# Optimization experiments

Measured on AMD Instinct MI355X. Metric: run time of the kernel, lower is better.

Reference implementation:

```python
import jax, jax.numpy as jnp
import numpy as np

N_NODES = 10000
N_EDGES = 320000
IN_DIM = 128
HID = 256


def setup_inputs() -> dict:
    key = jax.random.key(0)
    ks = jax.random.split(key, 10)
    s_in = 1.0 / np.sqrt(IN_DIM)
    s_h = 1.0 / np.sqrt(HID)
    return {
        "x": jax.random.normal(ks[0], (N_NODES, IN_DIM), dtype=jnp.float32),
        "edge_index": jax.random.randint(ks[1], (2, N_EDGES), 0, N_NODES, dtype=jnp.int64),
        # feature_projector Linear(IN_DIM -> HID)
        "Wp": jax.random.uniform(ks[2], (IN_DIM, HID), jnp.float32, -s_in, s_in),
        "bp": jax.random.uniform(ks[3], (HID,), jnp.float32, -s_in, s_in),
        # LSTM(input=HID, hidden=HID) params, torch layout [4H, H], gate order i,f,g,o
        "W_ih": jax.random.uniform(ks[4], (4 * HID, HID), jnp.float32, -s_h, s_h),
        "W_hh": jax.random.uniform(ks[5], (4 * HID, HID), jnp.float32, -s_h, s_h),
        "b_ih": jax.random.uniform(ks[6], (4 * HID,), jnp.float32, -s_h, s_h),
        "b_hh": jax.random.uniform(ks[7], (4 * HID,), jnp.float32, -s_h, s_h),
        # EvolveGCN-O initial weight [H, H] (glorot-style)
        "initial_weight": jax.random.normal(ks[8], (HID, HID), dtype=jnp.float32) * np.sqrt(2.0 / (2 * HID)),
        # GCNConv bias
        "b_gcn": jnp.zeros((HID,), dtype=jnp.float32),
    }


def _forward(x, edge_index, Wp, bp, W_ih, W_hh, b_ih, b_hh, initial_weight, b_gcn):
    n = x.shape[0]
    # 1) feature projection
    h = x @ Wp + bp  # [N, H]
    # 2) EvolveGCN-O: one LSTM step on the weight matrix (rows = batch),
    #    with h0 = c0 = initial_weight; evolved hidden state is the GCN weight.
    gates = initial_weight @ W_ih.T + b_ih + initial_weight @ W_hh.T + b_hh  # [H, 4H]
    i_g, f_g, g_g, o_g = jnp.split(gates, 4, axis=-1)
    c = jax.nn.sigmoid(f_g) * initial_weight + jax.nn.sigmoid(i_g) * jnp.tanh(g_g)
    W = jax.nn.sigmoid(o_g) * jnp.tanh(c)  # [H, H]
    # 3) GCN propagation with fixed W: out = D^{-1/2}(A+I)D^{-1/2} (h W) + b
    hw = h @ W  # [N, H]
    self_loop = jnp.arange(n, dtype=edge_index.dtype)
    src = jnp.concatenate([edge_index[0], self_loop])
    dst = jnp.concatenate([edge_index[1], self_loop])
    ones = jnp.ones(src.shape[0], dtype=hw.dtype)
    deg = jax.ops.segment_sum(ones, dst, num_segments=n)  # in-degree incl. self loop
    dinv = jnp.where(deg > 0, jax.lax.rsqrt(deg), 0.0)
    norm = dinv[src] * dinv[dst]  # [E+N]
    out = jax.ops.segment_sum(hw[src] * norm[:, None], dst, num_segments=n)
    return out + b_gcn


def reference(x, edge_index, Wp, bp, W_ih, W_hh, b_ih, b_hh, initial_weight, b_gcn):
    return _forward(x, edge_index, Wp, bp, W_ih, W_hh, b_ih, b_hh, initial_weight, b_gcn)
```

## Files before the change

### kernel.cpp

```cpp
#include <hip/hip_runtime.h>
#include <math.h>

#define N_NODES 10000
#define N_EDGES 320000
#define IN_DIM  128
#define HID     256
#define CAP     128

#define NB_GATES 128
#define NB_FILL  313
#define NB_XCVT  80

typedef __attribute__((ext_vector_type(8))) short frag_ab;
typedef __attribute__((ext_vector_type(4))) float frag_cd;


__device__ __forceinline__ unsigned bf16rne(float f) {
    union { float f; unsigned u; } c; c.f = f;
    return (c.u + 0x7FFFu + ((c.u >> 16) & 1u)) >> 16;
}

__global__ __launch_bounds__(256)
void k_prep(const int* __restrict__ ei, int* __restrict__ cursor,
            int* __restrict__ bucket, const float* __restrict__ iw,
            const float* __restrict__ wih, const float* __restrict__ whh,
            float* __restrict__ G) {
    __shared__ float smem[6144];
    if (blockIdx.x >= NB_GATES) {
        int e = ((blockIdx.x - NB_GATES) * 256 + threadIdx.x) * 4;
        if (e + 3 < N_EDGES) {
            int4 s4 = *(const int4*)&ei[e];
            int4 d4 = *(const int4*)&ei[N_EDGES + e];
            int p0 = atomicAdd(&cursor[d4.x], 1);
            if (p0 < CAP) bucket[d4.x * CAP + p0] = s4.x;
            int p1 = atomicAdd(&cursor[d4.y], 1);
            if (p1 < CAP) bucket[d4.y * CAP + p1] = s4.y;
            int p2 = atomicAdd(&cursor[d4.z], 1);
            if (p2 < CAP) bucket[d4.z * CAP + p2] = s4.z;
            int p3 = atomicAdd(&cursor[d4.w], 1);
            if (p3 < CAP) bucket[d4.w * CAP + p3] = s4.w;
        } else {
            for (int q = e; q < N_EDGES; ++q) {
                int s = ei[q];
                int d = ei[N_EDGES + q];
                int pos = atomicAdd(&cursor[d], 1);
                if (pos < CAP) bucket[d * CAP + pos] = s;
            }
        }
        return;
    }
    int bid = blockIdx.x;
    int m0 = (bid & 7) * 32, n0 = (bid >> 3) * 64;
    float (*aT)[32] = (float(*)[32])smem;
    float (*bS)[64] = (float(*)[64])(smem + 2048);
    int t = threadIdx.x;
    int tm = t & 15, tn = t >> 4;
    float acc[2][4] = {};
    for (int kt = 0; kt < 4; ++kt) {
        int k0 = kt * 64;
        {
            int row = t >> 3;
            #pragma unroll
            for (int r = 0; r < 2; ++r) {
                int kq = 2 * (t & 7) + r;
                float4 av = *(const float4*)&iw[(m0 + row) * HID + k0 + 4 * kq];
                aT[4 * kq + 0][row] = av.x; aT[4 * kq + 1][row] = av.y;
                aT[4 * kq + 2][row] = av.z; aT[4 * kq + 3][row] = av.w;
            }
        }
        {
            int row = t >> 2;
            #pragma unroll
            for (int r = 0; r < 4; ++r) {
                int kq = 4 * (t & 3) + r;
                float4 b1 = *(const float4*)&wih[(n0 + row) * HID + k0 + 4 * kq];
                float4 b2 = *(const float4*)&whh[(n0 + row) * HID + k0 + 4 * kq];
                bS[4 * kq + 0][row] = b1.x + b2.x; bS[4 * kq + 1][row] = b1.y + b2.y;
                bS[4 * kq + 2][row] = b1.z + b2.z; bS[4 * kq + 3][row] = b1.w + b2.w;
            }
        }
        __syncthreads();
        #pragma unroll 8
        for (int kk = 0; kk < 64; ++kk) {
            float2 a2 = *(const float2*)&aT[kk][2 * tm];
            float4 b4 = *(const float4*)&bS[kk][4 * tn];
            float a[2] = {a2.x, a2.y};
            float b[4] = {b4.x, b4.y, b4.z, b4.w};
            #pragma unroll
            for (int i = 0; i < 2; ++i)
                #pragma unroll
                for (int j = 0; j < 4; ++j)
                    acc[i][j] = fmaf(a[i], b[j], acc[i][j]);
        }
        __syncthreads();
    }
    #pragma unroll
    for (int i = 0; i < 2; ++i) {
        float4 o = make_float4(acc[i][0], acc[i][1], acc[i][2], acc[i][3]);
        *(float4*)&G[(m0 + 2 * tm + i) * 1024 + n0 + 4 * tn] = o;
    }
}

__device__ __forceinline__ float sig_f(float x)  { return 1.f / (1.f + __expf(-x)); }
__device__ __forceinline__ float tanh_f(float x) { return 1.f - 2.f / (1.f + __expf(2.f * x)); }

__global__ __launch_bounds__(256)
void k_wev_dinv_xcvt(const float* __restrict__ G, const float* __restrict__ iw,
                     const float* __restrict__ b_ih, const float* __restrict__ b_hh,
                     float* __restrict__ Wev, const int* __restrict__ cursor,
                     float* __restrict__ dinv, const float* __restrict__ x,
                     unsigned* __restrict__ xb) {
    if (blockIdx.x >= 296) {
        int tid = (blockIdx.x - 296) * 256 + threadIdx.x;
        const float2* x2 = (const float2*)x;
        #pragma unroll
        for (int it = 0; it < 32; ++it) {
            int idx = tid + it * (NB_XCVT * 256);
            if (idx < N_NODES * 64) {
                int v = idx >> 6;
                float dv = rsqrtf((float)(cursor[v] + 1));
                float2 val = x2[idx];
                xb[idx] = bf16rne(dv * val.x) | (bf16rne(dv * val.y) << 16);
            }
        }
        return;
    }
    if (blockIdx.x >= 256) {
        int v = (blockIdx.x - 256) * 256 + threadIdx.x;
        if (v < N_NODES) dinv[v] = rsqrtf((float)(cursor[v] + 1));
        return;
    }
    int r = blockIdx.x;
    int j = threadIdx.x;
    float gi = G[r * 1024 + 0   + j] + b_ih[0   + j] + b_hh[0   + j];
    float gf = G[r * 1024 + 256 + j] + b_ih[256 + j] + b_hh[256 + j];
    float gg = G[r * 1024 + 512 + j] + b_ih[512 + j] + b_hh[512 + j];
    float go = G[r * 1024 + 768 + j] + b_ih[768 + j] + b_hh[768 + j];
    float c  = sig_f(gf) * iw[r * HID + j] + sig_f(gi) * tanh_f(gg);
    Wev[r * HID + j] = sig_f(go) * tanh_f(c);
}

__global__ __launch_bounds__(256)
void k_wc_agg(const unsigned* __restrict__ xb, const int* __restrict__ bucket,
              const int* __restrict__ cursor, const float* __restrict__ dinv,
              unsigned* __restrict__ yb, float* __restrict__ rs,
              const float* __restrict__ Wp, const float* __restrict__ bp,
              const float* __restrict__ Wev, unsigned* __restrict__ wct,
              float* __restrict__ bc) {
    __shared__ float arow[HID];
    if (blockIdx.x < 129) {
        int a = blockIdx.x;
        int j = threadIdx.x;
        const float* srcRow = (a < IN_DIM) ? &Wp[a * HID] : bp;
        arow[j] = srcRow[j];
        __syncthreads();
        float acc = 0.f;
        #pragma unroll 4
        for (int k = 0; k < HID; ++k)
            acc = fmaf(arow[k], Wev[k * HID + j], acc);
        if (a < IN_DIM)
            ((unsigned short*)wct)[j * IN_DIM + a] = (unsigned short)bf16rne(acc);
        else
            bc[j] = acc;
        return;
    }
    int wv   = threadIdx.x >> 6;
    int lane = threadIdx.x & 63;
    int v = (blockIdx.x - 129) * 4 + wv;
    int cntv = cursor[v];
    float dv = dinv[v];
    int cnt = cntv > CAP ? CAP : cntv;
    unsigned self = xb[v * 64 + lane];
    union { unsigned u; float f; } c0, c1;
    c0.u = self << 16; c1.u = self & 0xFFFF0000u;
    float acc0 = c0.f, acc1 = c1.f;
    float wsum = dv;
    const int4* bkt4 = (const int4*)&bucket[v * CAP];
    int j = 0;
    for (; j + 4 <= cnt; j += 4) {
        int4 s = bkt4[j >> 2];
        float w0 = dinv[s.x], w1 = dinv[s.y], w2 = dinv[s.z], w3 = dinv[s.w];
        unsigned r0 = xb[s.x * 64 + lane];
        unsigned r1 = xb[s.y * 64 + lane];
        unsigned r2 = xb[s.z * 64 + lane];
        unsigned r3 = xb[s.w * 64 + lane];
        union { unsigned u; float f; } a0, a1;
        a0.u = r0 << 16; a1.u = r0 & 0xFFFF0000u; acc0 += a0.f; acc1 += a1.f;
        a0.u = r1 << 16; a1.u = r1 & 0xFFFF0000u; acc0 += a0.f; acc1 += a1.f;
        a0.u = r2 << 16; a1.u = r2 & 0xFFFF0000u; acc0 += a0.f; acc1 += a1.f;
        a0.u = r3 << 16; a1.u = r3 & 0xFFFF0000u; acc0 += a0.f; acc1 += a1.f;
        wsum += w0 + w1 + w2 + w3;
    }
    for (; j < cnt; ++j) {
        int s = ((const int*)bkt4)[j];
        wsum += dinv[s];
        unsigned r = xb[s * 64 + lane];
        union { unsigned u; float f; } a0, a1;
        a0.u = r << 16; a1.u = r & 0xFFFF0000u; acc0 += a0.f; acc1 += a1.f;
    }
    yb[v * 64 + lane] = bf16rne(dv * acc0) | (bf16rne(dv * acc1) << 16);
    if (lane == 0) rs[v] = dv * wsum;
}

__global__ __launch_bounds__(256)
void k_out(const unsigned* __restrict__ yb, const unsigned* __restrict__ wct,
           const float* __restrict__ bc, const float* __restrict__ rs,
           const float* __restrict__ b_gcn, float* __restrict__ out) {
    __shared__ float sm[32][260];
    int m0 = blockIdx.x * 32;
    int w = threadIdx.x >> 6, lane = threadIdx.x & 63;
    int q = lane >> 4, ln = lane & 15;
    const int4* yb4  = (const int4*)yb;
    const int4* wct4 = (const int4*)wct;
    union F { int4 v; frag_ab f; };
    F a[2][4];
    #pragma unroll
    for (int mt = 0; mt < 2; ++mt)
        #pragma unroll
        for (int kc = 0; kc < 4; ++kc)
            a[mt][kc].v = yb4[(m0 + mt * 16 + ln) * 16 + kc * 4 + q];
    #pragma unroll
    for (int i = 0; i < 4; ++i) {
        int n0w = w * 64 + i * 16;
        F b[4];
        #pragma unroll
        for (int kc = 0; kc < 4; ++kc)
            b[kc].v = wct4[(n0w + ln) * 16 + kc * 4 + q];
        frag_cd acc0 = {0.f, 0.f, 0.f, 0.f};
        frag_cd acc1 = {0.f, 0.f, 0.f, 0.f};
        #pragma unroll
        for (int kc = 0; kc < 4; ++kc) {
            acc0 = __builtin_amdgcn_mfma_f32_16x16x32_bf16(a[0][kc].f, b[kc].f, acc0, 0, 0, 0);
            acc1 = __builtin_amdgcn_mfma_f32_16x16x32_bf16(a[1][kc].f, b[kc].f, acc1, 0, 0, 0);
        }
        #pragma unroll
        for (int r = 0; r < 4; ++r) {
            sm[q * 4 + r][n0w + ln]      = acc0[r];
            sm[16 + q * 4 + r][n0w + ln] = acc1[r];
        }
    }
    __syncthreads();
    int m  = threadIdx.x >> 3;
    int cg = threadIdx.x & 7;
    int gm = m0 + m;
    if (gm < N_NODES) {
        float rsv = rs[gm];
        #pragma unroll
        for (int c = 0; c < 8; ++c) {
            int col = c * 32 + cg * 4;
            float4 vv  = *(float4*)&sm[m][col];
            float4 bcv = *(const float4*)&bc[col];
            float4 bgv = *(const float4*)&b_gcn[col];
            float4 o;
            o.x = vv.x + rsv * bcv.x + bgv.x;
            o.y = vv.y + rsv * bcv.y + bgv.y;
            o.z = vv.z + rsv * bcv.z + bgv.z;
            o.w = vv.w + rsv * bcv.w + bgv.w;
            *(float4*)&out[gm * HID + col] = o;
        }
    }
}

extern "C" void kernel_launch(void* const* d_in, const int* in_sizes, int n_in,
                              void* d_out, int out_size, void* d_ws, size_t ws_size,
                              hipStream_t stream) {
    const float* x     = (const float*)d_in[0];
    const int*   ei    = (const int*)d_in[1];
    const float* Wp    = (const float*)d_in[2];
    const float* bp    = (const float*)d_in[3];
    const float* W_ih  = (const float*)d_in[4];
    const float* W_hh  = (const float*)d_in[5];
    const float* b_ih  = (const float*)d_in[6];
    const float* b_hh  = (const float*)d_in[7];
    const float* iw    = (const float*)d_in[8];
    const float* b_gcn = (const float*)d_in[9];
    float* out = (float*)d_out;

    char* ws = (char*)d_ws;
    unsigned* yb     = (unsigned*)(ws + 0);
    float*    G      = (float*)   (ws + 2560000);
    float*    Wev    = (float*)   (ws + 3608576);
    unsigned* wct    = (unsigned*)(ws + 3870720);
    float*    bc     = (float*)   (ws + 3936256);
    float*    rs     = (float*)   (ws + 3937280);
    unsigned* xb     = (unsigned*)(ws + 3977280);
    int*      cursor = (int*)     (ws + 6537280);
    float*    dinv   = (float*)   (ws + 6577280);
    int*      bucket = (int*)     (ws + 6617280);

    hipMemsetAsync(cursor, 0, N_NODES * sizeof(int), stream);

    k_prep<<<NB_GATES + NB_FILL, 256, 0, stream>>>(ei, cursor, bucket, iw, W_ih, W_hh, G);
    k_wev_dinv_xcvt<<<256 + 40 + NB_XCVT, 256, 0, stream>>>(
        G, iw, b_ih, b_hh, Wev, cursor, dinv, x, xb);
    k_wc_agg<<<129 + 2500, 256, 0, stream>>>(xb, bucket, cursor, dinv, yb, rs, Wp, bp, Wev, wct, bc);
    k_out<<<313, 256, 0, stream>>>(yb, wct, bc, rs, b_gcn, out);
}
```

Before: 143.7 us.

## Split gate GEMM over K, move x bf16 conversion into prep kernel

The LSTM gate GEMM is split into two K-halves across twice as many blocks, writing partial sums to G and G2, which the Wev kernel then adds. The x-to-bf16 conversion no longer depends on degree, so it moves into the first kernel alongside edge bucketing and runs with many more blocks. The per-source dinv weighting shifts into the aggregation loop as FMAs. This shortens the critical path of the second kernel and spreads work across more CUs, at the cost of an extra partial-sum buffer and one extra multiply per gathered element.

```diff
diff --git a/kernel.cpp b/kernel.cpp
--- a/kernel.cpp
+++ b/kernel.cpp
@@ -7,9 +7,9 @@
 #define HID     256
 #define CAP     128
 
-#define NB_GATES 128
+#define NB_GATES 256
 #define NB_FILL  313
-#define NB_XCVT  80
+#define NB_XCVT  640
 
 typedef __attribute__((ext_vector_type(8))) short frag_ab;
 typedef __attribute__((ext_vector_type(4))) float frag_cd;
@@ -24,8 +24,22 @@
 void k_prep(const int* __restrict__ ei, int* __restrict__ cursor,
             int* __restrict__ bucket, const float* __restrict__ iw,
             const float* __restrict__ wih, const float* __restrict__ whh,
-            float* __restrict__ G) {
+            float* __restrict__ G, float* __restrict__ G2,
+            const float* __restrict__ x, unsigned* __restrict__ xb) {
     __shared__ float smem[6144];
+    if (blockIdx.x >= NB_GATES + NB_FILL) {
+        int tid = (blockIdx.x - NB_GATES - NB_FILL) * 256 + threadIdx.x;
+        const float2* x2 = (const float2*)x;
+        #pragma unroll
+        for (int it = 0; it < 4; ++it) {
+            int idx = tid + it * (NB_XCVT * 256);
+            if (idx < N_NODES * 64) {
+                float2 v = x2[idx];
+                xb[idx] = bf16rne(v.x) | (bf16rne(v.y) << 16);
+            }
+        }
+        return;
+    }
     if (blockIdx.x >= NB_GATES) {
         int e = ((blockIdx.x - NB_GATES) * 256 + threadIdx.x) * 4;
         if (e + 3 < N_EDGES) {
@@ -49,15 +63,18 @@
         }
         return;
     }
-    int bid = blockIdx.x;
-    int m0 = (bid & 7) * 32, n0 = (bid >> 3) * 64;
+    int half = blockIdx.x >> 7;
+    int sub  = blockIdx.x & 127;
+    int m0 = (sub & 7) * 32, n0 = (sub >> 3) * 64;
+    int kbase = half * 128;
+    float* Gh = half ? G2 : G;
     float (*aT)[32] = (float(*)[32])smem;
     float (*bS)[64] = (float(*)[64])(smem + 2048);
     int t = threadIdx.x;
     int tm = t & 15, tn = t >> 4;
     float acc[2][4] = {};
-    for (int kt = 0; kt < 4; ++kt) {
-        int k0 = kt * 64;
+    for (int kt = 0; kt < 2; ++kt) {
+        int k0 = kbase + kt * 64;
         {
             int row = t >> 3;
             #pragma unroll
@@ -97,7 +114,7 @@
     #pragma unroll
     for (int i = 0; i < 2; ++i) {
         float4 o = make_float4(acc[i][0], acc[i][1], acc[i][2], acc[i][3]);
-        *(float4*)&G[(m0 + 2 * tm + i) * 1024 + n0 + 4 * tn] = o;
+        *(float4*)&Gh[(m0 + 2 * tm + i) * 1024 + n0 + 4 * tn] = o;
     }
 }
 
@@ -105,26 +122,10 @@
 __device__ __forceinline__ float tanh_f(float x) { return 1.f - 2.f / (1.f + __expf(2.f * x)); }
 
 __global__ __launch_bounds__(256)
-void k_wev_dinv_xcvt(const float* __restrict__ G, const float* __restrict__ iw,
-                     const float* __restrict__ b_ih, const float* __restrict__ b_hh,
-                     float* __restrict__ Wev, const int* __restrict__ cursor,
-                     float* __restrict__ dinv, const float* __restrict__ x,
-                     unsigned* __restrict__ xb) {
-    if (blockIdx.x >= 296) {
-        int tid = (blockIdx.x - 296) * 256 + threadIdx.x;
-        const float2* x2 = (const float2*)x;
-        #pragma unroll
-        for (int it = 0; it < 32; ++it) {
-            int idx = tid + it * (NB_XCVT * 256);
-            if (idx < N_NODES * 64) {
-                int v = idx >> 6;
-                float dv = rsqrtf((float)(cursor[v] + 1));
-                float2 val = x2[idx];
-                xb[idx] = bf16rne(dv * val.x) | (bf16rne(dv * val.y) << 16);
-            }
-        }
-        return;
-    }
+void k_wev_dinv(const float* __restrict__ G, const float* __restrict__ G2,
+                const float* __restrict__ iw, const float* __restrict__ b_ih,
+                const float* __restrict__ b_hh, float* __restrict__ Wev,
+                const int* __restrict__ cursor, float* __restrict__ dinv) {
     if (blockIdx.x >= 256) {
         int v = (blockIdx.x - 256) * 256 + threadIdx.x;
         if (v < N_NODES) dinv[v] = rsqrtf((float)(cursor[v] + 1));
@@ -132,10 +133,10 @@
     }
     int r = blockIdx.x;
     int j = threadIdx.x;
-    float gi = G[r * 1024 + 0   + j] + b_ih[0   + j] + b_hh[0   + j];
-    float gf = G[r * 1024 + 256 + j] + b_ih[256 + j] + b_hh[256 + j];
-    float gg = G[r * 1024 + 512 + j] + b_ih[512 + j] + b_hh[512 + j];
-    float go = G[r * 1024 + 768 + j] + b_ih[768 + j] + b_hh[768 + j];
+    float gi = G[r * 1024 + 0   + j] + G2[r * 1024 + 0   + j] + b_ih[0   + j] + b_hh[0   + j];
+    float gf = G[r * 1024 + 256 + j] + G2[r * 1024 + 256 + j] + b_ih[256 + j] + b_hh[256 + j];
+    float gg = G[r * 1024 + 512 + j] + G2[r * 1024 + 512 + j] + b_ih[512 + j] + b_hh[512 + j];
+    float go = G[r * 1024 + 768 + j] + G2[r * 1024 + 768 + j] + b_ih[768 + j] + b_hh[768 + j];
     float c  = sig_f(gf) * iw[r * HID + j] + sig_f(gi) * tanh_f(gg);
     Wev[r * HID + j] = sig_f(go) * tanh_f(c);
 }
@@ -173,7 +174,7 @@
     unsigned self = xb[v * 64 + lane];
     union { unsigned u; float f; } c0, c1;
     c0.u = self << 16; c1.u = self & 0xFFFF0000u;
-    float acc0 = c0.f, acc1 = c1.f;
+    float acc0 = dv * c0.f, acc1 = dv * c1.f;
     float wsum = dv;
     const int4* bkt4 = (const int4*)&bucket[v * CAP];
     int j = 0;
@@ -185,18 +186,24 @@
         unsigned r2 = xb[s.z * 64 + lane];
         unsigned r3 = xb[s.w * 64 + lane];
         union { unsigned u; float f; } a0, a1;
-        a0.u = r0 << 16; a1.u = r0 & 0xFFFF0000u; acc0 += a0.f; acc1 += a1.f;
-        a0.u = r1 << 16; a1.u = r1 & 0xFFFF0000u; acc0 += a0.f; acc1 += a1.f;
-        a0.u = r2 << 16; a1.u = r2 & 0xFFFF0000u; acc0 += a0.f; acc1 += a1.f;
-        a0.u = r3 << 16; a1.u = r3 & 0xFFFF0000u; acc0 += a0.f; acc1 += a1.f;
+        a0.u = r0 << 16; a1.u = r0 & 0xFFFF0000u;
+        acc0 = fmaf(w0, a0.f, acc0); acc1 = fmaf(w0, a1.f, acc1);
+        a0.u = r1 << 16; a1.u = r1 & 0xFFFF0000u;
+        acc0 = fmaf(w1, a0.f, acc0); acc1 = fmaf(w1, a1.f, acc1);
+        a0.u = r2 << 16; a1.u = r2 & 0xFFFF0000u;
+        acc0 = fmaf(w2, a0.f, acc0); acc1 = fmaf(w2, a1.f, acc1);
+        a0.u = r3 << 16; a1.u = r3 & 0xFFFF0000u;
+        acc0 = fmaf(w3, a0.f, acc0); acc1 = fmaf(w3, a1.f, acc1);
         wsum += w0 + w1 + w2 + w3;
     }
     for (; j < cnt; ++j) {
         int s = ((const int*)bkt4)[j];
-        wsum += dinv[s];
+        float w = dinv[s];
         unsigned r = xb[s * 64 + lane];
         union { unsigned u; float f; } a0, a1;
-        a0.u = r << 16; a1.u = r & 0xFFFF0000u; acc0 += a0.f; acc1 += a1.f;
+        a0.u = r << 16; a1.u = r & 0xFFFF0000u;
+        acc0 = fmaf(w, a0.f, acc0); acc1 = fmaf(w, a1.f, acc1);
+        wsum += w;
     }
     yb[v * 64 + lane] = bf16rne(dv * acc0) | (bf16rne(dv * acc1) << 16);
     if (lane == 0) rs[v] = dv * wsum;
@@ -279,20 +286,21 @@
     char* ws = (char*)d_ws;
     unsigned* yb     = (unsigned*)(ws + 0);
     float*    G      = (float*)   (ws + 2560000);
-    float*    Wev    = (float*)   (ws + 3608576);
-    unsigned* wct    = (unsigned*)(ws + 3870720);
-    float*    bc     = (float*)   (ws + 3936256);
-    float*    rs     = (float*)   (ws + 3937280);
-    unsigned* xb     = (unsigned*)(ws + 3977280);
-    int*      cursor = (int*)     (ws + 6537280);
-    float*    dinv   = (float*)   (ws + 6577280);
-    int*      bucket = (int*)     (ws + 6617280);
+    float*    G2     = (float*)   (ws + 3608576);
+    float*    Wev    = (float*)   (ws + 4657152);
+    unsigned* wct    = (unsigned*)(ws + 4919296);
+    float*    bc     = (float*)   (ws + 4984832);
+    float*    rs     = (float*)   (ws + 4985856);
+    unsigned* xb     = (unsigned*)(ws + 5025856);
+    int*      cursor = (int*)     (ws + 7585856);
+    float*    dinv   = (float*)   (ws + 7625856);
+    int*      bucket = (int*)     (ws + 7665856);
 
     hipMemsetAsync(cursor, 0, N_NODES * sizeof(int), stream);
 
-    k_prep<<<NB_GATES + NB_FILL, 256, 0, stream>>>(ei, cursor, bucket, iw, W_ih, W_hh, G);
-    k_wev_dinv_xcvt<<<256 + 40 + NB_XCVT, 256, 0, stream>>>(
-        G, iw, b_ih, b_hh, Wev, cursor, dinv, x, xb);
+    k_prep<<<NB_GATES + NB_FILL + NB_XCVT, 256, 0, stream>>>(
+        ei, cursor, bucket, iw, W_ih, W_hh, G, G2, x, xb);
+    k_wev_dinv<<<256 + 40, 256, 0, stream>>>(G, G2, iw, b_ih, b_hh, Wev, cursor, dinv);
     k_wc_agg<<<129 + 2500, 256, 0, stream>>>(xb, bucket, cursor, dinv, yb, rs, Wp, bp, Wev, wct, bc);
     k_out<<<313, 256, 0, stream>>>(yb, wct, bc, rs, b_gcn, out);
 }
```

Result: faster. 135.3 us (-5.9%).
